# Kernel tuning notes

Measured on AMD Instinct MI355X. Metric: run time of the kernel, lower is better.

Reference implementation:

```python
import jax, jax.numpy as jnp
import numpy as np

B, V, E = 2, 50000, 400000
FIN, COND, HID, OUT, ENC, EDG = 128, 32, 256, 128, 64, 16
EPS = 1e-5


def setup_inputs() -> dict:
    key = jax.random.key(0)
    ks = jax.random.split(key, 24)
    rn = lambda k, shp, s=0.05: jax.random.normal(k, shp, jnp.float32) * s
    return {
        "x": jax.random.normal(ks[0], (B, V, FIN), jnp.float32),
        "cond_x": jax.random.normal(ks[1], (V, COND), jnp.float32),
        "edge_attr": jax.random.normal(ks[2], (E, EDG), jnp.float32),
        "t": jax.random.normal(ks[3], (B, ENC), jnp.float32),
        "edge_index": jax.random.randint(ks[4], (2, E), 0, V, dtype=jnp.int32),
        # GCNConv weights (in, hid) + bias; Linear weights (hid, out) + bias
        "w_c0": rn(ks[5], (FIN + COND, HID)), "b_c0": rn(ks[6], (HID,)),
        "w_l0": rn(ks[7], (HID, HID)), "b_l0": rn(ks[8], (HID,)),
        "w_c1": rn(ks[9], (HID, HID)), "b_c1": rn(ks[10], (HID,)),
        "w_l1": rn(ks[11], (HID, HID)), "b_l1": rn(ks[12], (HID,)),
        "w_c2": rn(ks[13], (HID, HID)), "b_c2": rn(ks[14], (HID,)),
        "w_l2": rn(ks[15], (HID, OUT)), "b_l2": rn(ks[16], (OUT,)),
        "gn_g": jnp.ones((HID,), jnp.float32), "gn_b": jnp.zeros((HID,), jnp.float32),
        "film_w": rn(ks[17], (ENC, 2 * HID)), "film_b": rn(ks[18], (2 * HID,)),
    }


def _gcn(h, src, dst, dinv, W, b):
    # GCNConv: symmetric-normalized aggregation with self loops, then +bias.
    hw = h @ W  # (B, V, H)
    coef = (dinv[src] * dinv[dst])[None, :, None]            # (1, E, 1)
    self_loop = hw * (dinv * dinv)[None, :, None]            # norm of (i,i) edge
    agg = self_loop.at[:, dst, :].add(hw[:, src, :] * coef)  # scatter-add over dst
    return agg + b


def _groupnorm1(h, gamma, beta):
    # nn.GroupNorm(1, C) applied to (B, C, V): normalize over (C, V) per sample.
    mu = h.mean(axis=(1, 2), keepdims=True)
    var = ((h - mu) ** 2).mean(axis=(1, 2), keepdims=True)
    return (h - mu) * jax.lax.rsqrt(var + EPS) * gamma + beta


def reference(x, cond_x, edge_attr, t, edge_index,
              w_c0, b_c0, w_l0, b_l0, w_c1, b_c1, w_l1, b_l1,
              w_c2, b_c2, w_l2, b_l2, gn_g, gn_b, film_w, film_b):
    src, dst = edge_index[0], edge_index[1]
    deg = jnp.ones((V,), jnp.float32).at[dst].add(1.0)  # 1 = self loop
    dinv = jax.lax.rsqrt(deg)

    x_skip = x
    cond = jnp.broadcast_to(cond_x[None], (x.shape[0], V, COND))
    h = jnp.concatenate([x, cond], axis=-1)  # (B, V, FIN+COND)

    # layer 0: feature dim != hidden -> no norm
    h = jax.nn.relu(_gcn(h, src, dst, dinv, w_c0, b_c0))
    h = jax.nn.relu(h @ w_l0 + b_l0)  # dropout p=0 -> identity

    # layer 1: GroupNorm(1, hidden) then conv/linear
    h = _groupnorm1(h, gn_g, gn_b)
    h = jax.nn.relu(_gcn(h, src, dst, dinv, w_c1, b_c1))
    h = jax.nn.relu(h @ w_l1 + b_l1)

    # final gconv + FiLM + relu + linear + residual
    h = _gcn(h, src, dst, dinv, w_c2, b_c2)
    gb = t @ film_w + film_b                 # (B, 2*HID)
    gamma, beta = gb[:, :HID], gb[:, HID:]
    h = h * gamma[:, None, :] + beta[:, None, :]
    h = jax.nn.relu(h)
    out = h @ w_l2 + b_l2 + x_skip
    return out
```

## Files before the change

kernel.cpp:

```cpp
#include <hip/hip_runtime.h>
#include <stdint.h>

typedef unsigned short u16;
typedef short bf16x8 __attribute__((ext_vector_type(8)));
typedef float f32x4 __attribute__((ext_vector_type(4)));
typedef unsigned int u32x4 __attribute__((ext_vector_type(4)));

constexpr int B_ = 2, V_ = 50000, E_ = 400000;
constexpr int FIN_ = 128, COND_ = 32, HID_ = 256, OUT_ = 128, ENC_ = 64;
constexpr int M_ = B_ * V_;
constexpr int MP_ = M_ + 256;
constexpr int K0_ = FIN_ + COND_;
constexpr float EPS_ = 1e-5f;

#define DEV static __device__ __forceinline__

DEV float b2f(u16 u) { union { float f; uint32_t i; } x; x.i = ((uint32_t)u) << 16; return x.f; }
DEV u16 f2b(float f) {
  union { float f; uint32_t i; } x; x.f = f;
  uint32_t r = x.i + 0x7fffu + ((x.i >> 16) & 1u);
  return (u16)(r >> 16);
}
DEV uint32_t pk2(float a, float b) { return (uint32_t)f2b(a) | ((uint32_t)f2b(b) << 16); }

#define GLDS16(gp, lp) __builtin_amdgcn_global_load_lds( \
    (const __attribute__((address_space(1))) void*)(gp), \
    (__attribute__((address_space(3))) void*)(lp), 16, 0, 0)

__global__ void k_count(const int* __restrict__ dst, int* __restrict__ cnt) {
  int e = blockIdx.x * blockDim.x + threadIdx.x;
  if (e < E_) atomicAdd(&cnt[dst[e]], 1);
}

__global__ void k_dinv(const int* __restrict__ cnt, float* __restrict__ dinv) {
  int v = blockIdx.x * blockDim.x + threadIdx.x;
  if (v < V_) dinv[v] = rsqrtf(1.0f + (float)cnt[v]);
}

__global__ __launch_bounds__(1024) void k_scan1(const int* __restrict__ cnt,
                                                int* __restrict__ tmp, int* __restrict__ bsum) {
  __shared__ int s[1024];
  int tid = threadIdx.x;
  int i = blockIdx.x * 1024 + tid;
  int v = (i < V_) ? cnt[i] : 0;
  s[tid] = v;
  __syncthreads();
  for (int off = 1; off < 1024; off <<= 1) {
    int t = (tid >= off) ? s[tid - off] : 0;
    __syncthreads();
    s[tid] += t;
    __syncthreads();
  }
  if (i < V_) tmp[i] = s[tid];
  if (tid == 1023) bsum[blockIdx.x] = s[1023];
}

__global__ void k_scan2(int* __restrict__ bsum, int n) {
  if (threadIdx.x == 0) {
    int a = 0;
    for (int i = 0; i < n; ++i) { a += bsum[i]; bsum[i] = a; }
  }
}

__global__ void k_scan3(const int* __restrict__ cnt, const int* __restrict__ tmp,
                        const int* __restrict__ bsum, int* __restrict__ row_ptr,
                        int* __restrict__ cursor) {
  int i = blockIdx.x * blockDim.x + threadIdx.x;
  if (i >= V_) return;
  int blk = i >> 10;
  int offs = blk ? bsum[blk - 1] : 0;
  int incl = tmp[i] + offs;
  row_ptr[i + 1] = incl;
  cursor[i] = incl - cnt[i];
  if (i == 0) row_ptr[0] = 0;
}

__global__ void k_fill(const int* __restrict__ src, const int* __restrict__ dst,
                       const float* __restrict__ dinv,
                       int* __restrict__ cursor, int2* __restrict__ csr) {
  int e = blockIdx.x * blockDim.x + threadIdx.x;
  if (e < E_) {
    int s = src[e], d = dst[e];
    int p = atomicAdd(&cursor[d], 1);
    float cf = dinv[s] * dinv[d];
    csr[p] = make_int2(s, __float_as_int(cf));
  }
}

__global__ void k_rowsum(const float* __restrict__ dinv, const int* __restrict__ row_ptr,
                         const int2* __restrict__ csr, float* __restrict__ rowsum) {
  int v = blockIdx.x * blockDim.x + threadIdx.x;
  if (v >= V_) return;
  float dv = dinv[v];
  float s = dv * dv;
  int e = row_ptr[v + 1];
  for (int j = row_ptr[v]; j < e; ++j) s += __int_as_float(csr[j].y);
  rowsum[v] = s;
}

__global__ void k_film(const float* __restrict__ t, const float* __restrict__ fw,
                       const float* __restrict__ fb, float* __restrict__ gb) {
  int b = blockIdx.x; int j = threadIdx.x;
  float acc = fb[j];
  for (int k = 0; k < ENC_; ++k) acc += t[b * ENC_ + k] * fw[k * 512 + j];
  gb[b * 512 + j] = acc;
}

__global__ void k_wconv(const float* __restrict__ W, u16* __restrict__ WT, int K, int N) {
  int idx = blockIdx.x * blockDim.x + threadIdx.x;
  if (idx < K * N) {
    int k = idx / N, n = idx % N;
    WT[n * K + k] = f2b(W[idx]);
  }
}

__global__ void k_wconv_g(const float* __restrict__ W, const float* __restrict__ gng,
                          u16* __restrict__ WT, int K, int N) {
  int idx = blockIdx.x * blockDim.x + threadIdx.x;
  if (idx < K * N) {
    int k = idx / N, n = idx % N;
    WT[n * K + k] = f2b(W[idx] * gng[k]);
  }
}

__global__ void k_gnreduce(const float4* __restrict__ part, int nblk,
                           float* __restrict__ stats) {
  int tid = threadIdx.x;
  float s0 = 0.f, ss0 = 0.f, s1 = 0.f, ss1 = 0.f;
  for (int i = tid; i < nblk; i += 256) {
    float4 p = part[i];
    s0 += p.x; ss0 += p.y; s1 += p.z; ss1 += p.w;
  }
  __shared__ float red[4][4];
#pragma unroll
  for (int o = 32; o > 0; o >>= 1) {
    s0  += __shfl_down(s0, o, 64);
    ss0 += __shfl_down(ss0, o, 64);
    s1  += __shfl_down(s1, o, 64);
    ss1 += __shfl_down(ss1, o, 64);
  }
  int w = tid >> 6, ln = tid & 63;
  if (ln == 0) { red[w][0] = s0; red[w][1] = ss0; red[w][2] = s1; red[w][3] = ss1; }
  __syncthreads();
  if (tid == 0) {
    float S0 = red[0][0] + red[1][0] + red[2][0] + red[3][0];
    float SS0 = red[0][1] + red[1][1] + red[2][1] + red[3][1];
    float S1 = red[0][2] + red[1][2] + red[2][2] + red[3][2];
    float SS1 = red[0][3] + red[1][3] + red[2][3] + red[3][3];
    float n = (float)V_ * (float)HID_;
    float mu0 = S0 / n, var0 = SS0 / n - mu0 * mu0;
    float mu1 = S1 / n, var1 = SS1 / n - mu1 * mu1;
    stats[0] = mu0; stats[1] = rsqrtf(var0 + EPS_);
    stats[2] = mu1; stats[3] = rsqrtf(var1 + EPS_);
  }
}

__global__ void k_gnfold(const float* __restrict__ gng, const float* __restrict__ gnb,
                         const float* __restrict__ W, const float* __restrict__ stats,
                         float* __restrict__ kc) {
  int n = blockIdx.x, c = threadIdx.x;
  float wv = W[c * HID_ + n];
  float gw = gng[c] * wv, bw = gnb[c] * wv;
  __shared__ float sg[4], sb[4];
#pragma unroll
  for (int o = 32; o > 0; o >>= 1) {
    gw += __shfl_down(gw, o, 64);
    bw += __shfl_down(bw, o, 64);
  }
  int w = c >> 6, ln = c & 63;
  if (ln == 0) { sg[w] = gw; sb[w] = bw; }
  __syncthreads();
  if (c == 0) {
    float G = sg[0] + sg[1] + sg[2] + sg[3];
    float Bw = sb[0] + sb[1] + sb[2] + sb[3];
    for (int b = 0; b < B_; ++b)
      kc[b * HID_ + n] = Bw - stats[b * 2] * stats[b * 2 + 1] * G;
  }
}

__global__ void k_prep0(const float* __restrict__ x, const float* __restrict__ cond,
                        u16* __restrict__ A0) {
  int idx = blockIdx.x * blockDim.x + threadIdx.x;
  if (idx >= M_ * K0_ / 4) return;
  int e = idx * 4;
  int r = e / K0_, c = e % K0_;
  f32x4 v;
  if (c < FIN_) v = __builtin_nontemporal_load((const f32x4*)&x[(size_t)r * FIN_ + c]);
  else { int vv = r % V_; v = *(const f32x4*)&cond[(size_t)vv * COND_ + (c - FIN_)]; }
  uint2 o;
  o.x = pk2(v[0], v[1]);
  o.y = pk2(v[2], v[3]);
  *(uint2*)&A0[e] = o;
}

template<int KW>
__global__ __launch_bounds__(256) void k_gather(
    const u16* __restrict__ hw, const float* __restrict__ dinv,
    const int* __restrict__ row_ptr, const int2* __restrict__ csr,
    u16* __restrict__ out)
{
  __shared__ f32x4 redA[3][2][32];
  __shared__ f32x4 redB[3][2][32];
  const int v   = blockIdx.x;
  const int tid = threadIdx.x;
  const int nb  = tid >> 6;
  const int b   = (tid >> 5) & 1;
  const int l   = tid & 31;
  const int c0  = l * 8;
  const bool act = l < (KW / 8);

  const float dv = dinv[v];
  const int beg = row_ptr[v], end = row_ptr[v + 1];

  float acc[8];
#pragma unroll
  for (int k = 0; k < 8; ++k) acc[k] = 0.f;

  if (act) {
    int j = beg + nb;
    for (; j + 4 < end; j += 8) {
      int2 e0 = csr[j];
      int2 e1 = csr[j + 4];
      float cf0 = __int_as_float(e0.y);
      float cf1 = __int_as_float(e1.y);
      uint4 u0 = *(const uint4*)&hw[((size_t)b * V_ + e0.x) * KW + c0];
      uint4 u1 = *(const uint4*)&hw[((size_t)b * V_ + e1.x) * KW + c0];
      u16 a0[8]; *(uint4*)a0 = u0;
      u16 a1[8]; *(uint4*)a1 = u1;
#pragma unroll
      for (int k = 0; k < 8; ++k) acc[k] += b2f(a0[k]) * cf0;
#pragma unroll
      for (int k = 0; k < 8; ++k) acc[k] += b2f(a1[k]) * cf1;
    }
    if (j < end) {
      int2 e0 = csr[j];
      float cf0 = __int_as_float(e0.y);
      uint4 u0 = *(const uint4*)&hw[((size_t)b * V_ + e0.x) * KW + c0];
      u16 a0[8]; *(uint4*)a0 = u0;
#pragma unroll
      for (int k = 0; k < 8; ++k) acc[k] += b2f(a0[k]) * cf0;
    }
  }

  if (nb > 0) {
    redA[nb - 1][b][l] = f32x4{acc[0], acc[1], acc[2], acc[3]};
    redB[nb - 1][b][l] = f32x4{acc[4], acc[5], acc[6], acc[7]};
  }
  __syncthreads();
  if (nb == 0 && act) {
#pragma unroll
    for (int g = 0; g < 3; ++g) {
      f32x4 ra = redA[g][b][l], rb = redB[g][b][l];
      acc[0] += ra[0]; acc[1] += ra[1]; acc[2] += ra[2]; acc[3] += ra[3];
      acc[4] += rb[0]; acc[5] += rb[1]; acc[6] += rb[2]; acc[7] += rb[3];
    }
    float sl = dv * dv;
    uint4 u = *(const uint4*)&hw[((size_t)b * V_ + v) * KW + c0];
    u16 us[8]; *(uint4*)us = u;
#pragma unroll
    for (int k = 0; k < 8; ++k) acc[k] += b2f(us[k]) * sl;
    u32x4 o;
    o[0] = pk2(acc[0], acc[1]);
    o[1] = pk2(acc[2], acc[3]);
    o[2] = pk2(acc[4], acc[5]);
    o[3] = pk2(acc[6], acc[7]);
    __builtin_nontemporal_store(o, (u32x4*)&out[((size_t)b * V_ + v) * KW + c0]);
  }
}

template<int P1E, int P2E, int K1, int N2>
__global__ __launch_bounds__(256) void k_pair(
    const u16* __restrict__ A, const u16* __restrict__ W1T, const u16* __restrict__ W2T,
    const float* __restrict__ b1, const float* __restrict__ b2,
    const float* __restrict__ stats, const float* __restrict__ kc,
    const float* __restrict__ rowsum, const float* __restrict__ gb,
    const float* __restrict__ xres, float4* __restrict__ part,
    void* __restrict__ Out)
{
  constexpr int BM = 64, BK = 32, N1 = 256;
  constexpr int FN2 = N2 / 64;
  __shared__ alignas(16) u16 Asg[BM * BK];
  __shared__ alignas(16) u16 Bsg[N1 * BK];
  __shared__ alignas(16) u16 T1[BM * N1];
  __shared__ float sred[4][4];
  const int tile_m = blockIdx.x * BM;
  const int tid = threadIdx.x;
  const int wave = tid >> 6, lane = tid & 63;
  const int lr = lane & 15, lkg = lane >> 4;
  const int phys = lkg ^ ((lr >> 1) & 3);

  f32x4 acc[4][4];
#pragma unroll
  for (int i = 0; i < 4; ++i)
#pragma unroll
    for (int j = 0; j < 4; ++j) acc[i][j] = {0.f, 0.f, 0.f, 0.f};

  for (int kb = 0; kb < K1; kb += BK) {
    {
      int row = tid >> 2;
      int sslot = (tid & 3) ^ ((row >> 1) & 3);
      GLDS16(A + (size_t)(tile_m + row) * K1 + kb + sslot * 8, &Asg[(wave * 64) * 8]);
    }
#pragma unroll
    for (int it = 0; it < 4; ++it) {
      int c = tid + it * 256;
      int row = c >> 2;
      int sslot = (c & 3) ^ ((row >> 1) & 3);
      GLDS16(W1T + (size_t)row * K1 + kb + sslot * 8, &Bsg[(it * 256 + wave * 64) * 8]);
    }
    __syncthreads();
    bf16x8 af[4], bf[4];
#pragma unroll
    for (int fm = 0; fm < 4; ++fm) af[fm] = *(const bf16x8*)&Asg[(fm * 16 + lr) * BK + phys * 8];
#pragma unroll
    for (int fn = 0; fn < 4; ++fn) bf[fn] = *(const bf16x8*)&Bsg[(wave * 64 + fn * 16 + lr) * BK + phys * 8];
#pragma unroll
    for (int fm = 0; fm < 4; ++fm)
#pragma unroll
      for (int fn = 0; fn < 4; ++fn)
        acc[fm][fn] = __builtin_amdgcn_mfma_f32_16x16x32_bf16(bf[fn], af[fm], acc[fm][fn], 0, 0, 0);
    __syncthreads();
  }

#pragma unroll
  for (int fm = 0; fm < 4; ++fm) {
    const int row = fm * 16 + lr;
    const int gr = tile_m + row;
    const int bb = (gr >= V_) ? 1 : 0;
    float rsc = 1.f, rsum = 0.f;
    if (P1E == 1) {
      rsc = stats[bb * 2 + 1];
      int node = (gr < M_) ? (gr - bb * V_) : 0;
      rsum = rowsum[node];
    }
#pragma unroll
    for (int fn = 0; fn < 4; ++fn) {
      const int colb = wave * 64 + fn * 16 + lkg * 4;
      float v0 = acc[fm][fn][0], v1 = acc[fm][fn][1];
      float v2 = acc[fm][fn][2], v3 = acc[fm][fn][3];
      float4 bs = *(const float4*)&b1[colb];
      if (P1E == 0) {
        v0 = fmaxf(v0 + bs.x, 0.f); v1 = fmaxf(v1 + bs.y, 0.f);
        v2 = fmaxf(v2 + bs.z, 0.f); v3 = fmaxf(v3 + bs.w, 0.f);
      }
      if (P1E == 1) {
        float4 kcv = *(const float4*)&kc[bb * 256 + colb];
        v0 = fmaxf(v0 * rsc + rsum * kcv.x + bs.x, 0.f);
        v1 = fmaxf(v1 * rsc + rsum * kcv.y + bs.y, 0.f);
        v2 = fmaxf(v2 * rsc + rsum * kcv.z + bs.z, 0.f);
        v3 = fmaxf(v3 * rsc + rsum * kcv.w + bs.w, 0.f);
      }
      if (P1E == 2) {
        float4 g = *(const float4*)&gb[bb * 512 + colb];
        float4 be = *(const float4*)&gb[bb * 512 + 256 + colb];
        v0 = fmaxf((v0 + bs.x) * g.x + be.x, 0.f);
        v1 = fmaxf((v1 + bs.y) * g.y + be.y, 0.f);
        v2 = fmaxf((v2 + bs.z) * g.z + be.z, 0.f);
        v3 = fmaxf((v3 + bs.w) * g.w + be.w, 0.f);
      }
      int pg = (colb >> 2) ^ ((row & 7) << 1);
      uint2 o; o.x = pk2(v0, v1); o.y = pk2(v2, v3);
      *(uint2*)&T1[row * 256 + pg * 4] = o;
    }
  }
  __syncthreads();

  f32x4 acc2[4][FN2];
#pragma unroll
  for (int i = 0; i < 4; ++i)
#pragma unroll
    for (int j = 0; j < FN2; ++j) acc2[i][j] = {0.f, 0.f, 0.f, 0.f};

  for (int kb2 = 0; kb2 < 256; kb2 += BK) {
#pragma unroll
    for (int it = 0; it < FN2; ++it) {
      int c = tid + it * 256;
      int row = c >> 2;
      int sslot = (c & 3) ^ ((row >> 1) & 3);
      GLDS16(W2T + (size_t)row * 256 + kb2 + sslot * 8, &Bsg[(it * 256 + wave * 64) * 8]);
    }
    __syncthreads();
    bf16x8 af2[4], bf2[FN2];
#pragma unroll
    for (int fm = 0; fm < 4; ++fm) {
      int row = fm * 16 + lr;
      int pg = ((kb2 >> 2) + lkg * 2) ^ ((row & 7) << 1);
      af2[fm] = *(const bf16x8*)&T1[row * 256 + pg * 4];
    }
#pragma unroll
    for (int fn = 0; fn < FN2; ++fn)
      bf2[fn] = *(const bf16x8*)&Bsg[(wave * (N2 / 4) + fn * 16 + lr) * BK + phys * 8];
#pragma unroll
    for (int fm = 0; fm < 4; ++fm)
#pragma unroll
      for (int fn = 0; fn < FN2; ++fn)
        acc2[fm][fn] = __builtin_amdgcn_mfma_f32_16x16x32_bf16(bf2[fn], af2[fm], acc2[fm][fn], 0, 0, 0);
    __syncthreads();
  }

  float s0 = 0.f, ss0 = 0.f, s1 = 0.f, ss1 = 0.f;
#pragma unroll
  for (int fm = 0; fm < 4; ++fm) {
    const int row = tile_m + fm * 16 + lr;
    if (row >= M_) continue;
#pragma unroll
    for (int fn = 0; fn < FN2; ++fn) {
      const int colb = wave * (N2 / 4) + fn * 16 + lkg * 4;
      float v0 = acc2[fm][fn][0], v1 = acc2[fm][fn][1];
      float v2 = acc2[fm][fn][2], v3 = acc2[fm][fn][3];
      float4 bs = *(const float4*)&b2[colb];
      if (P2E == 0 || P2E == 1) {
        v0 = fmaxf(v0 + bs.x, 0.f); v1 = fmaxf(v1 + bs.y, 0.f);
        v2 = fmaxf(v2 + bs.z, 0.f); v3 = fmaxf(v3 + bs.w, 0.f);
        if (P2E == 1) {
          if (row >= V_) { s1 += v0 + v1 + v2 + v3; ss1 += v0*v0 + v1*v1 + v2*v2 + v3*v3; }
          else           { s0 += v0 + v1 + v2 + v3; ss0 += v0*v0 + v1*v1 + v2*v2 + v3*v3; }
        }
        uint2 o; o.x = pk2(v0, v1); o.y = pk2(v2, v3);
        *(uint2*)&((u16*)Out)[(size_t)row * N2 + colb] = o;
      } else {
        f32x4 xr = __builtin_nontemporal_load((const f32x4*)&xres[(size_t)row * N2 + colb]);
        f32x4 o;
        o[0] = v0 + bs.x + xr[0]; o[1] = v1 + bs.y + xr[1];
        o[2] = v2 + bs.z + xr[2]; o[3] = v3 + bs.w + xr[3];
        __builtin_nontemporal_store(o, (f32x4*)&((float*)Out)[(size_t)row * N2 + colb]);
      }
    }
  }
  if (P2E == 1) {
#pragma unroll
    for (int o = 32; o > 0; o >>= 1) {
      s0  += __shfl_down(s0, o, 64);
      ss0 += __shfl_down(ss0, o, 64);
      s1  += __shfl_down(s1, o, 64);
      ss1 += __shfl_down(ss1, o, 64);
    }
    if (lane == 0) { sred[wave][0] = s0; sred[wave][1] = ss0; sred[wave][2] = s1; sred[wave][3] = ss1; }
    __syncthreads();
    if (tid == 0) {
      float4 p;
      p.x = sred[0][0] + sred[1][0] + sred[2][0] + sred[3][0];
      p.y = sred[0][1] + sred[1][1] + sred[2][1] + sred[3][1];
      p.z = sred[0][2] + sred[1][2] + sred[2][2] + sred[3][2];
      p.w = sred[0][3] + sred[1][3] + sred[2][3] + sred[3][3];
      part[blockIdx.x] = p;
    }
  }
}

extern "C" void kernel_launch(void* const* d_in, const int* in_sizes, int n_in,
                              void* d_out, int out_size, void* d_ws, size_t ws_size,
                              hipStream_t stream) {
  (void)in_sizes; (void)n_in; (void)out_size; (void)ws_size;
  const float* x      = (const float*)d_in[0];
  const float* cond_x = (const float*)d_in[1];
  const float* t      = (const float*)d_in[3];
  const int*   ei     = (const int*)d_in[4];
  const float* w_c0 = (const float*)d_in[5];  const float* b_c0 = (const float*)d_in[6];
  const float* w_l0 = (const float*)d_in[7];  const float* b_l0 = (const float*)d_in[8];
  const float* w_c1 = (const float*)d_in[9];  const float* b_c1 = (const float*)d_in[10];
  const float* w_l1 = (const float*)d_in[11]; const float* b_l1 = (const float*)d_in[12];
  const float* w_c2 = (const float*)d_in[13]; const float* b_c2 = (const float*)d_in[14];
  const float* w_l2 = (const float*)d_in[15]; const float* b_l2 = (const float*)d_in[16];
  const float* gn_g = (const float*)d_in[17]; const float* gn_b = (const float*)d_in[18];
  const float* film_w = (const float*)d_in[19]; const float* film_b = (const float*)d_in[20];

  char* wsp = (char*)d_ws;
  size_t off = 0;
  auto alloc = [&](size_t bytes) -> char* {
    char* p = wsp + off; off += (bytes + 255) & ~(size_t)255; return p;
  };
  constexpr int GM64 = (M_ + 63) / 64;
  int*   cnt       = (int*)  alloc((size_t)V_ * 4);
  int*   row_ptr   = (int*)  alloc((size_t)(V_ + 1) * 4);
  int*   cursor    = (int*)  alloc((size_t)V_ * 4);
  int2*  csr       = (int2*) alloc((size_t)E_ * 8);
  int*   scan_tmp  = (int*)  alloc((size_t)V_ * 4);
  int*   scan_bsum = (int*)  alloc(64 * 4);
  float* dinv      = (float*)alloc((size_t)V_ * 4);
  float* rowsum    = (float*)alloc((size_t)V_ * 4);
  float* stats     = (float*)alloc(16);
  float4* part     = (float4*)alloc((size_t)GM64 * 16);
  float* gb        = (float*)alloc(2 * 512 * 4);
  float* kc        = (float*)alloc(2 * HID_ * 4);
  u16* wc0T  = (u16*)alloc((size_t)256 * 160 * 2);
  u16* wl0T  = (u16*)alloc((size_t)256 * 256 * 2);
  u16* wc1Tg = (u16*)alloc((size_t)256 * 256 * 2);
  u16* wl1T  = (u16*)alloc((size_t)256 * 256 * 2);
  u16* wc2T  = (u16*)alloc((size_t)256 * 256 * 2);
  u16* wl2T  = (u16*)alloc((size_t)128 * 256 * 2);
  u16* A0    = (u16*)alloc((size_t)MP_ * K0_ * 2);
  u16* HA0   = (u16*)alloc((size_t)MP_ * K0_ * 2);
  u16* HB    = (u16*)alloc((size_t)MP_ * HID_ * 2);
  u16* HA1   = (u16*)alloc((size_t)MP_ * HID_ * 2);

  const int* srcI = ei;
  const int* dstI = ei + E_;

  hipMemsetAsync(cnt, 0, (size_t)V_ * 4, stream);

  constexpr int NBLK = (V_ + 1023) / 1024;
  k_count<<<dim3((E_ + 255) / 256), dim3(256), 0, stream>>>(dstI, cnt);
  k_dinv <<<dim3((V_ + 255) / 256), dim3(256), 0, stream>>>(cnt, dinv);
  k_scan1<<<dim3(NBLK), dim3(1024), 0, stream>>>(cnt, scan_tmp, scan_bsum);
  k_scan2<<<dim3(1), dim3(64), 0, stream>>>(scan_bsum, NBLK);
  k_scan3<<<dim3((V_ + 255) / 256), dim3(256), 0, stream>>>(cnt, scan_tmp, scan_bsum, row_ptr, cursor);
  k_fill <<<dim3((E_ + 255) / 256), dim3(256), 0, stream>>>(srcI, dstI, dinv, cursor, csr);
  k_rowsum<<<dim3((V_ + 255) / 256), dim3(256), 0, stream>>>(dinv, row_ptr, csr, rowsum);
  k_film <<<dim3(2), dim3(512), 0, stream>>>(t, film_w, film_b, gb);

  k_wconv  <<<dim3((160 * 256 + 255) / 256), dim3(256), 0, stream>>>(w_c0, wc0T, 160, 256);
  k_wconv  <<<dim3((256 * 256 + 255) / 256), dim3(256), 0, stream>>>(w_l0, wl0T, 256, 256);
  k_wconv_g<<<dim3((256 * 256 + 255) / 256), dim3(256), 0, stream>>>(w_c1, gn_g, wc1Tg, 256, 256);
  k_wconv  <<<dim3((256 * 256 + 255) / 256), dim3(256), 0, stream>>>(w_l1, wl1T, 256, 256);
  k_wconv  <<<dim3((256 * 256 + 255) / 256), dim3(256), 0, stream>>>(w_c2, wc2T, 256, 256);
  k_wconv  <<<dim3((256 * 128 + 255) / 256), dim3(256), 0, stream>>>(w_l2, wl2T, 256, 128);

  k_prep0<<<dim3(M_ * K0_ / 4 / 256), dim3(256), 0, stream>>>(x, cond_x, A0);

  k_gather<160><<<dim3(V_), 256, 0, stream>>>(A0, dinv, row_ptr, csr, HA0);
  k_pair<0, 1, 160, 256><<<dim3(GM64), 256, 0, stream>>>(
      HA0, wc0T, wl0T, b_c0, b_l0, nullptr, nullptr, nullptr, nullptr, nullptr, part, HB);

  k_gnreduce<<<dim3(1), dim3(256), 0, stream>>>(part, GM64, stats);
  k_gnfold <<<dim3(256), dim3(256), 0, stream>>>(gn_g, gn_b, w_c1, stats, kc);

  k_gather<256><<<dim3(V_), 256, 0, stream>>>(HB, dinv, row_ptr, csr, HA1);
  k_pair<1, 0, 256, 256><<<dim3(GM64), 256, 0, stream>>>(
      HA1, wc1Tg, wl1T, b_c1, b_l1, stats, kc, rowsum, nullptr, nullptr, nullptr, HB);

  k_gather<256><<<dim3(V_), 256, 0, stream>>>(HB, dinv, row_ptr, csr, HA1);
  k_pair<2, 2, 256, 128><<<dim3(GM64), 256, 0, stream>>>(
      HA1, wc2T, wl2T, b_c2, b_l2, nullptr, nullptr, nullptr, gb, x, nullptr, (void*)d_out);
}
```

Measured before the change: 525.1 us.

## Fuse neighbor gather into per-tile GEMM pair kernel

Removes the standalone per-node gather kernels and instead has each GEMM tile block aggregate its 64 rows' neighbors directly into shared memory before the first matmul. This eliminates writing and re-reading the aggregated activation buffer for each layer and saves kernel launches. In exchange the gather runs with one thread per row-quarter looping serially over edges, with large per-thread accumulators and less memory-level parallelism. Shared memory is consolidated into one tile buffer reused for both matmul stages.

```diff
diff --git a/kernel.cpp b/kernel.cpp
--- a/kernel.cpp
+++ b/kernel.cpp
@@ -4,7 +4,6 @@
 typedef unsigned short u16;
 typedef short bf16x8 __attribute__((ext_vector_type(8)));
 typedef float f32x4 __attribute__((ext_vector_type(4)));
-typedef unsigned int u32x4 __attribute__((ext_vector_type(4)));
 
 constexpr int B_ = 2, V_ = 50000, E_ = 400000;
 constexpr int FIN_ = 128, COND_ = 32, HID_ = 256, OUT_ = 128, ENC_ = 64;
@@ -193,84 +192,11 @@
   *(uint2*)&A0[e] = o;
 }
 
-template<int KW>
-__global__ __launch_bounds__(256) void k_gather(
+template<int P1E, int P2E, int K1, int N2>
+__global__ __launch_bounds__(256) void k_mega(
     const u16* __restrict__ hw, const float* __restrict__ dinv,
     const int* __restrict__ row_ptr, const int2* __restrict__ csr,
-    u16* __restrict__ out)
-{
-  __shared__ f32x4 redA[3][2][32];
-  __shared__ f32x4 redB[3][2][32];
-  const int v   = blockIdx.x;
-  const int tid = threadIdx.x;
-  const int nb  = tid >> 6;
-  const int b   = (tid >> 5) & 1;
-  const int l   = tid & 31;
-  const int c0  = l * 8;
-  const bool act = l < (KW / 8);
-
-  const float dv = dinv[v];
-  const int beg = row_ptr[v], end = row_ptr[v + 1];
-
-  float acc[8];
-#pragma unroll
-  for (int k = 0; k < 8; ++k) acc[k] = 0.f;
-
-  if (act) {
-    int j = beg + nb;
-    for (; j + 4 < end; j += 8) {
-      int2 e0 = csr[j];
-      int2 e1 = csr[j + 4];
-      float cf0 = __int_as_float(e0.y);
-      float cf1 = __int_as_float(e1.y);
-      uint4 u0 = *(const uint4*)&hw[((size_t)b * V_ + e0.x) * KW + c0];
-      uint4 u1 = *(const uint4*)&hw[((size_t)b * V_ + e1.x) * KW + c0];
-      u16 a0[8]; *(uint4*)a0 = u0;
-      u16 a1[8]; *(uint4*)a1 = u1;
-#pragma unroll
-      for (int k = 0; k < 8; ++k) acc[k] += b2f(a0[k]) * cf0;
-#pragma unroll
-      for (int k = 0; k < 8; ++k) acc[k] += b2f(a1[k]) * cf1;
-    }
-    if (j < end) {
-      int2 e0 = csr[j];
-      float cf0 = __int_as_float(e0.y);
-      uint4 u0 = *(const uint4*)&hw[((size_t)b * V_ + e0.x) * KW + c0];
-      u16 a0[8]; *(uint4*)a0 = u0;
-#pragma unroll
-      for (int k = 0; k < 8; ++k) acc[k] += b2f(a0[k]) * cf0;
-    }
-  }
-
-  if (nb > 0) {
-    redA[nb - 1][b][l] = f32x4{acc[0], acc[1], acc[2], acc[3]};
-    redB[nb - 1][b][l] = f32x4{acc[4], acc[5], acc[6], acc[7]};
-  }
-  __syncthreads();
-  if (nb == 0 && act) {
-#pragma unroll
-    for (int g = 0; g < 3; ++g) {
-      f32x4 ra = redA[g][b][l], rb = redB[g][b][l];
-      acc[0] += ra[0]; acc[1] += ra[1]; acc[2] += ra[2]; acc[3] += ra[3];
-      acc[4] += rb[0]; acc[5] += rb[1]; acc[6] += rb[2]; acc[7] += rb[3];
-    }
-    float sl = dv * dv;
-    uint4 u = *(const uint4*)&hw[((size_t)b * V_ + v) * KW + c0];
-    u16 us[8]; *(uint4*)us = u;
-#pragma unroll
-    for (int k = 0; k < 8; ++k) acc[k] += b2f(us[k]) * sl;
-    u32x4 o;
-    o[0] = pk2(acc[0], acc[1]);
-    o[1] = pk2(acc[2], acc[3]);
-    o[2] = pk2(acc[4], acc[5]);
-    o[3] = pk2(acc[6], acc[7]);
-    __builtin_nontemporal_store(o, (u32x4*)&out[((size_t)b * V_ + v) * KW + c0]);
-  }
-}
-
-template<int P1E, int P2E, int K1, int N2>
-__global__ __launch_bounds__(256) void k_pair(
-    const u16* __restrict__ A, const u16* __restrict__ W1T, const u16* __restrict__ W2T,
+    const u16* __restrict__ W1T, const u16* __restrict__ W2T,
     const float* __restrict__ b1, const float* __restrict__ b2,
     const float* __restrict__ stats, const float* __restrict__ kc,
     const float* __restrict__ rowsum, const float* __restrict__ gb,
@@ -279,9 +205,9 @@
 {
   constexpr int BM = 64, BK = 32, N1 = 256;
   constexpr int FN2 = N2 / 64;
-  __shared__ alignas(16) u16 Asg[BM * BK];
+  constexpr int NU = K1 / 32;
+  __shared__ alignas(16) u16 TA[BM * 256];
   __shared__ alignas(16) u16 Bsg[N1 * BK];
-  __shared__ alignas(16) u16 T1[BM * N1];
   __shared__ float sred[4][4];
   const int tile_m = blockIdx.x * BM;
   const int tid = threadIdx.x;
@@ -289,6 +215,56 @@
   const int lr = lane & 15, lkg = lane >> 4;
   const int phys = lkg ^ ((lr >> 1) & 3);
 
+  {
+    const int r = tid >> 2, q = tid & 3;
+    const int gr = tile_m + r;
+    const int c0 = q * (K1 / 4);
+    float av[NU * 8];
+#pragma unroll
+    for (int k = 0; k < NU * 8; ++k) av[k] = 0.f;
+    if (gr < M_) {
+      const int b = (gr >= V_) ? 1 : 0;
+      const int node = gr - b * V_;
+      const u16* __restrict__ hb = hw + (size_t)b * V_ * K1;
+      const int beg = row_ptr[node], end = row_ptr[node + 1];
+      for (int j = beg; j < end; ++j) {
+        int2 e = csr[j];
+        float cf = __int_as_float(e.y);
+        const u16* rp = hb + (size_t)e.x * K1 + c0;
+#pragma unroll
+        for (int u = 0; u < NU; ++u) {
+          uint4 ld = *(const uint4*)&rp[u * 8];
+          u16 us[8]; *(uint4*)us = ld;
+#pragma unroll
+          for (int k = 0; k < 8; ++k) av[u * 8 + k] += b2f(us[k]) * cf;
+        }
+      }
+      float dv = dinv[node];
+      float sl = dv * dv;
+      const u16* rp = hb + (size_t)node * K1 + c0;
+#pragma unroll
+      for (int u = 0; u < NU; ++u) {
+        uint4 ld = *(const uint4*)&rp[u * 8];
+        u16 us[8]; *(uint4*)us = ld;
+#pragma unroll
+        for (int k = 0; k < 8; ++k) av[u * 8 + k] += b2f(us[k]) * sl;
+      }
+    }
+    const int X = (r & 7) << 1;
+    const int cb = c0 >> 3;
+#pragma unroll
+    for (int u = 0; u < NU; ++u) {
+      int pg = (((cb + u) << 1) ^ X);
+      uint4 o;
+      o.x = pk2(av[u * 8 + 0], av[u * 8 + 1]);
+      o.y = pk2(av[u * 8 + 2], av[u * 8 + 3]);
+      o.z = pk2(av[u * 8 + 4], av[u * 8 + 5]);
+      o.w = pk2(av[u * 8 + 6], av[u * 8 + 7]);
+      *(uint4*)&TA[r * 256 + pg * 4] = o;
+    }
+  }
+  __syncthreads();
+
   f32x4 acc[4][4];
 #pragma unroll
   for (int i = 0; i < 4; ++i)
@@ -296,11 +272,6 @@
     for (int j = 0; j < 4; ++j) acc[i][j] = {0.f, 0.f, 0.f, 0.f};
 
   for (int kb = 0; kb < K1; kb += BK) {
-    {
-      int row = tid >> 2;
-      int sslot = (tid & 3) ^ ((row >> 1) & 3);
-      GLDS16(A + (size_t)(tile_m + row) * K1 + kb + sslot * 8, &Asg[(wave * 64) * 8]);
-    }
 #pragma unroll
     for (int it = 0; it < 4; ++it) {
       int c = tid + it * 256;
@@ -311,7 +282,11 @@
     __syncthreads();
     bf16x8 af[4], bf[4];
 #pragma unroll
-    for (int fm = 0; fm < 4; ++fm) af[fm] = *(const bf16x8*)&Asg[(fm * 16 + lr) * BK + phys * 8];
+    for (int fm = 0; fm < 4; ++fm) {
+      int row = fm * 16 + lr;
+      int pg = ((kb >> 2) + lkg * 2) ^ ((row & 7) << 1);
+      af[fm] = *(const bf16x8*)&TA[row * 256 + pg * 4];
+    }
 #pragma unroll
     for (int fn = 0; fn < 4; ++fn) bf[fn] = *(const bf16x8*)&Bsg[(wave * 64 + fn * 16 + lr) * BK + phys * 8];
 #pragma unroll
@@ -360,7 +335,7 @@
       }
       int pg = (colb >> 2) ^ ((row & 7) << 1);
       uint2 o; o.x = pk2(v0, v1); o.y = pk2(v2, v3);
-      *(uint2*)&T1[row * 256 + pg * 4] = o;
+      *(uint2*)&TA[row * 256 + pg * 4] = o;
     }
   }
   __syncthreads();
@@ -385,7 +360,7 @@
     for (int fm = 0; fm < 4; ++fm) {
       int row = fm * 16 + lr;
       int pg = ((kb2 >> 2) + lkg * 2) ^ ((row & 7) << 1);
-      af2[fm] = *(const bf16x8*)&T1[row * 256 + pg * 4];
+      af2[fm] = *(const bf16x8*)&TA[row * 256 + pg * 4];
     }
 #pragma unroll
     for (int fn = 0; fn < FN2; ++fn)
@@ -490,9 +465,8 @@
   u16* wc2T  = (u16*)alloc((size_t)256 * 256 * 2);
   u16* wl2T  = (u16*)alloc((size_t)128 * 256 * 2);
   u16* A0    = (u16*)alloc((size_t)MP_ * K0_ * 2);
-  u16* HA0   = (u16*)alloc((size_t)MP_ * K0_ * 2);
   u16* HB    = (u16*)alloc((size_t)MP_ * HID_ * 2);
-  u16* HA1   = (u16*)alloc((size_t)MP_ * HID_ * 2);
+  u16* HC    = (u16*)alloc((size_t)MP_ * HID_ * 2);
 
   const int* srcI = ei;
   const int* dstI = ei + E_;
@@ -518,18 +492,18 @@
 
   k_prep0<<<dim3(M_ * K0_ / 4 / 256), dim3(256), 0, stream>>>(x, cond_x, A0);
 
-  k_gather<160><<<dim3(V_), 256, 0, stream>>>(A0, dinv, row_ptr, csr, HA0);
-  k_pair<0, 1, 160, 256><<<dim3(GM64), 256, 0, stream>>>(
-      HA0, wc0T, wl0T, b_c0, b_l0, nullptr, nullptr, nullptr, nullptr, nullptr, part, HB);
+  k_mega<0, 1, 160, 256><<<dim3(GM64), 256, 0, stream>>>(
+      A0, dinv, row_ptr, csr, wc0T, wl0T, b_c0, b_l0,
+      nullptr, nullptr, nullptr, nullptr, nullptr, part, HB);
 
   k_gnreduce<<<dim3(1), dim3(256), 0, stream>>>(part, GM64, stats);
   k_gnfold <<<dim3(256), dim3(256), 0, stream>>>(gn_g, gn_b, w_c1, stats, kc);
 
-  k_gather<256><<<dim3(V_), 256, 0, stream>>>(HB, dinv, row_ptr, csr, HA1);
-  k_pair<1, 0, 256, 256><<<dim3(GM64), 256, 0, stream>>>(
-      HA1, wc1Tg, wl1T, b_c1, b_l1, stats, kc, rowsum, nullptr, nullptr, nullptr, HB);
-
-  k_gather<256><<<dim3(V_), 256, 0, stream>>>(HB, dinv, row_ptr, csr, HA1);
-  k_pair<2, 2, 256, 128><<<dim3(GM64), 256, 0, stream>>>(
-      HA1, wc2T, wl2T, b_c2, b_l2, nullptr, nullptr, nullptr, gb, x, nullptr, (void*)d_out);
-}
+  k_mega<1, 0, 256, 256><<<dim3(GM64), 256, 0, stream>>>(
+      HB, dinv, row_ptr, csr, wc1Tg, wl1T, b_c1, b_l1,
+      stats, kc, rowsum, nullptr, nullptr, nullptr, HC);
+
+  k_mega<2, 2, 256, 128><<<dim3(GM64), 256, 0, stream>>>(
+      HC, dinv, row_ptr, csr, wc2T, wl2T, b_c2, b_l2,
+      nullptr, nullptr, nullptr, gb, x, nullptr, (void*)d_out);
+}
```

Result: slower. 554.4 us (+5.6%).
